# Kernel tuning notes

Hardware: AMD Instinct MI355X
Metric: run time of the kernel (lower is better)

## Reference

```python
import math
import jax, jax.numpy as jnp
import numpy as np

EPS = 1e-5
NUM_HEADS = 8

def gelu(x):
    return jax.nn.gelu(x, approximate=False)  # keras 'gelu' is exact

def layernorm(x, g, b):
    m = jnp.mean(x, axis=-1, keepdims=True)
    v = jnp.var(x, axis=-1, keepdims=True)
    return (x - m) * jax.lax.rsqrt(v + EPS) * g + b

def setup_inputs() -> dict:
    key = jax.random.key(0)
    ks = jax.random.split(key, 12)
    B, S, N, D = 2, 1, 2048, 256
    E = 256  # dim_emb == dim_out
    s_in = 1.0 / np.sqrt(D).astype(np.float32)
    s_e = 1.0 / np.sqrt(E).astype(np.float32)
    s_h = 1.0 / np.sqrt(4 * E).astype(np.float32)
    return {
        "X": jax.random.normal(ks[0], (B, S, N, D), jnp.float32),
        "Wq": jax.random.normal(ks[1], (D, E), jnp.float32) * s_in,
        "Wk": jax.random.normal(ks[2], (D, E), jnp.float32) * s_in,
        "Wv": jax.random.normal(ks[3], (D, E), jnp.float32) * s_in,
        "Wm": jax.random.normal(ks[4], (E, E), jnp.float32) * s_e,
        "bm": jnp.zeros((E,), jnp.float32),
        "W1": jax.random.normal(ks[5], (E, 4 * E), jnp.float32) * s_e,
        "bf1": jnp.zeros((4 * E,), jnp.float32),
        "W2": jax.random.normal(ks[6], (4 * E, E), jnp.float32) * s_h,
        "bf2": jnp.zeros((E,), jnp.float32),
        "ln0_g": jnp.ones((D,), jnp.float32),
        "ln0_b": jnp.zeros((D,), jnp.float32),
        "ln1_g": jnp.ones((E,), jnp.float32),
        "ln1_b": jnp.zeros((E,), jnp.float32),
    }

def reference(X, Wq, Wk, Wv, Wm, bm, W1, bf1, W2, bf2, ln0_g, ln0_b, ln1_g, ln1_b):
    B, S, N, D = X.shape  # S == 1 (set-transformer singleton axis)
    E = Wq.shape[1]
    H = NUM_HEADS
    dh = E // H
    dim_KV = D  # softmax scale uses dim_KV, not head dim (faithful to source)

    # pre-layer-norm applies only to the Q branch; K/V use raw X
    Xn = layernorm(X, ln0_g, ln0_b)
    Q = Xn @ Wq                      # (B,1,N,E)
    K = X @ Wk
    V = X @ Wv
    X_res = Q                        # fc_res is None -> residual is Q

    def to_heads(T):                 # (B,1,N,E) -> (B,H,N,dh), split along last dim
        return T[:, 0].reshape(B, N, H, dh).transpose(0, 2, 1, 3)

    q, k, v = to_heads(Q), to_heads(K), to_heads(V)
    A = jnp.einsum('bhnd,bhmd->bhnm', q, k) * (1.0 / math.sqrt(dim_KV))  # (B,H,N,N)
    P = jax.nn.softmax(A, axis=-1)
    mh = jnp.einsum('bhnm,bhmd->bhnd', P, v)            # (B,H,N,dh)
    mh = mh.transpose(0, 2, 1, 3).reshape(B, 1, N, E)   # concat heads on last dim

    Hm = gelu(mh @ Wm + bm)          # fc_mix_heads has gelu activation
    H_after_res = Hm + X_res
    H_rff = layernorm(H_after_res, ln1_g, ln1_b)

    # rff: Dense(4E, gelu) then an extra explicit gelu, then Dense(E, gelu)
    h1 = gelu(gelu(H_rff @ W1 + bf1))
    h2 = gelu(h1 @ W2 + bf2)
    return H_after_res + h2
```

## Files before the change

### kernel.cpp

```cpp
#include <hip/hip_runtime.h>
#include <math.h>

#define NTOK 2048
#define EDIM 256
#define ROWS 4096
#define SLOT (ROWS * EDIM)

typedef __attribute__((ext_vector_type(8))) short bf16x8;
typedef __attribute__((ext_vector_type(4))) short bf16x4_t;
typedef __attribute__((ext_vector_type(4))) unsigned short u16x4;
typedef __attribute__((ext_vector_type(4))) float f32x4;
typedef __attribute__((ext_vector_type(4))) unsigned u32x4;
typedef __attribute__((ext_vector_type(2))) unsigned u32x2;

__device__ __forceinline__ float gelu_f(float x) {
    return 0.5f * x * (1.0f + erff(x * 0.70710678118654752f));
}
__device__ __forceinline__ unsigned short f2bf(float x) {
    unsigned u = __builtin_bit_cast(unsigned, x);
    u += 0x7FFFu + ((u >> 16) & 1u);
    return (unsigned short)(u >> 16);
}
__device__ __forceinline__ float bf2f(unsigned short h) {
    unsigned u = ((unsigned)h) << 16;
    return __builtin_bit_cast(float, u);
}
__device__ __forceinline__ unsigned pack2(float lo, float hi) {
    unsigned r;
    asm("v_cvt_pk_bf16_f32 %0, %1, %2" : "=v"(r) : "v"(lo), "v"(hi));
    return r;
}

__global__ __launch_bounds__(256) void trans_w(const float* __restrict__ Wq, const float* __restrict__ Wk,
                                               const float* __restrict__ Wv, const float* __restrict__ Wm,
                                               const float* __restrict__ W1, const float* __restrict__ W2,
                                               unsigned short* WqT, unsigned short* WkvT,
                                               unsigned short* WmT, unsigned short* W1T,
                                               unsigned short* W2T) {
    __shared__ float Ls[64][65];
    const int bid = blockIdx.x;
    const float* src;
    unsigned short* dst;
    int K, N, t;
    if (bid < 16)       { src = Wq; dst = WqT;             K = 256;  N = 256;  t = bid; }
    else if (bid < 32)  { src = Wk; dst = WkvT;            K = 256;  N = 256;  t = bid - 16; }
    else if (bid < 48)  { src = Wv; dst = WkvT + 256*256;  K = 256;  N = 256;  t = bid - 32; }
    else if (bid < 64)  { src = Wm; dst = WmT;             K = 256;  N = 256;  t = bid - 48; }
    else if (bid < 128) { src = W1; dst = W1T;             K = 256;  N = 1024; t = bid - 64; }
    else                { src = W2; dst = W2T;             K = 1024; N = 256;  t = bid - 128; }
    const int tn = N >> 6;
    const int k0 = (t / tn) * 64, n0 = (t % tn) * 64;
    const int r = threadIdx.x >> 2, cq = threadIdx.x & 3;
#pragma unroll
    for (int u = 0; u < 4; ++u) {
        const float4 v = *(const float4*)&src[(size_t)(k0 + r) * N + n0 + cq * 16 + u * 4];
        Ls[r][cq * 16 + u * 4 + 0] = v.x;
        Ls[r][cq * 16 + u * 4 + 1] = v.y;
        Ls[r][cq * 16 + u * 4 + 2] = v.z;
        Ls[r][cq * 16 + u * 4 + 3] = v.w;
    }
    __syncthreads();
#pragma unroll
    for (int hh = 0; hh < 2; ++hh) {
        bf16x8 o;
#pragma unroll
        for (int j = 0; j < 8; ++j) o[j] = (short)f2bf(Ls[cq * 16 + hh * 8 + j][r]);
        *(bf16x8*)&dst[(size_t)(n0 + r) * K + k0 + cq * 16 + hh * 8] = o;
    }
}

template <bool RAW>
__global__ __launch_bounds__(256) void ln_bf16(const float* __restrict__ X, const float* __restrict__ g,
                                               const float* __restrict__ b, unsigned short* __restrict__ Y,
                                               unsigned short* __restrict__ Yraw) {
    const int wave = threadIdx.x >> 6, lane = threadIdx.x & 63;
    const int row = blockIdx.x * 4 + wave;
    const float4 v = *(const float4*)&X[(size_t)row * EDIM + lane * 4];
    float s = v.x + v.y + v.z + v.w;
    float s2 = v.x * v.x + v.y * v.y + v.z * v.z + v.w * v.w;
#pragma unroll
    for (int off = 1; off < 64; off <<= 1) {
        s += __shfl_xor(s, off);
        s2 += __shfl_xor(s2, off);
    }
    const float mean = s * (1.0f / 256.0f);
    const float var = s2 * (1.0f / 256.0f) - mean * mean;
    const float rstd = rsqrtf(var + 1e-5f);
    const float4 gg = *(const float4*)&g[lane * 4];
    const float4 bb = *(const float4*)&b[lane * 4];
    u16x4 o;
    o[0] = f2bf((v.x - mean) * rstd * gg.x + bb.x);
    o[1] = f2bf((v.y - mean) * rstd * gg.y + bb.y);
    o[2] = f2bf((v.z - mean) * rstd * gg.z + bb.z);
    o[3] = f2bf((v.w - mean) * rstd * gg.w + bb.w);
    *(u16x4*)&Y[(size_t)row * EDIM + lane * 4] = o;
    if (RAW) {
        u16x4 rw;
        rw[0] = f2bf(v.x); rw[1] = f2bf(v.y); rw[2] = f2bf(v.z); rw[3] = f2bf(v.w);
        *(u16x4*)&Yraw[(size_t)row * EDIM + lane * 4] = rw;
    }
}

template <int EPI, int BN>
__global__ __launch_bounds__(256) void gemm_bf16(const unsigned short* __restrict__ A,
                                                 const unsigned short* __restrict__ Bt,
                                                 const float* __restrict__ bias,
                                                 const float* __restrict__ res,
                                                 float* __restrict__ outF,
                                                 unsigned short* __restrict__ outB,
                                                 int M, int N, int K) {
    constexpr int NI = BN / 32;
    __shared__ unsigned short As[32][72];
    __shared__ unsigned short Bs[BN][72];
    const int tid = threadIdx.x;
    const int lane = tid & 63, wid = tid >> 6;
    const int c = lane & 15, g = lane >> 4;
    const int wm = wid & 1, wn = wid >> 1;
    const int row0 = blockIdx.y * 32, col0 = blockIdx.x * BN;
    const int sarow = tid >> 3, saq = tid & 7;
    f32x4 acc[NI] = {};
    for (int k0 = 0; k0 < K; k0 += 64) {
        __syncthreads();
        {
            const bf16x8 a0 = *(const bf16x8*)&A[(size_t)(row0 + sarow) * K + k0 + saq * 8];
            *(bf16x8*)&As[sarow][saq * 8] = a0;
            if (BN == 64) {
                const int sbrow = tid >> 2, sbq = tid & 3;
                const bf16x8* gb = (const bf16x8*)&Bt[(size_t)(col0 + sbrow) * K + k0 + sbq * 16];
                const bf16x8 b0 = gb[0], b1 = gb[1];
                *(bf16x8*)&Bs[sbrow][sbq * 16] = b0;
                *(bf16x8*)&Bs[sbrow][sbq * 16 + 8] = b1;
            } else {
                const bf16x8 b0 = *(const bf16x8*)&Bt[(size_t)(col0 + sarow) * K + k0 + saq * 8];
                *(bf16x8*)&Bs[sarow][saq * 8] = b0;
            }
        }
        __syncthreads();
#pragma unroll
        for (int ks = 0; ks < 2; ++ks) {
            const bf16x8 af = *(const bf16x8*)&As[wm * 16 + c][ks * 32 + 8 * g];
#pragma unroll
            for (int ni = 0; ni < NI; ++ni) {
                const bf16x8 bv = *(const bf16x8*)&Bs[(wn * NI + ni) * 16 + c][ks * 32 + 8 * g];
                acc[ni] = __builtin_amdgcn_mfma_f32_16x16x32_bf16(af, bv, acc[ni], 0, 0, 0);
            }
        }
    }
#pragma unroll
    for (int ni = 0; ni < NI; ++ni) {
        const int colx = col0 + (wn * NI + ni) * 16 + c;
        const float bi = (EPI != 0) ? bias[colx] : 0.0f;
#pragma unroll
        for (int r = 0; r < 4; ++r) {
            const int rowx = row0 + wm * 16 + 4 * g + r;
            const size_t idx = (size_t)rowx * N + colx;
            float v = acc[ni][r];
            if (EPI == 1) v = res[idx] + gelu_f(v + bi);
            else if (EPI == 2) v = gelu_f(gelu_f(v + bi));
            if (outF) outF[idx] = v;
            if (outB) outB[idx] = f2bf(v);
        }
    }
}

__global__ __launch_bounds__(256) void attn_mfma(const unsigned short* __restrict__ Qb,
                                                 const unsigned short* __restrict__ KVb,
                                                 unsigned short* __restrict__ Opart,
                                                 float* __restrict__ ML) {
    __shared__ char smem[18944];
    unsigned short (*Ks)[64][40] = (unsigned short (*)[64][40])smem;
    unsigned short (*Vt)[32][68] = (unsigned short (*)[32][68])(smem + 10240);
    float (*Otf)[16][36]         = (float (*)[16][36])smem;
    const int tid = threadIdx.x, lane = tid & 63, wid = tid >> 6;
    const int c = lane & 15, g = lane >> 4;
    const int bid = blockIdx.x;
    const int qt = bid & 31, h = (bid >> 5) & 7, b = (bid >> 8) & 1, s = bid >> 9;
    const int qrow = b * NTOK + qt * 64 + wid * 16;
    const int skey = tid >> 2, skq = tid & 3;
    const int vkp = tid & 31, vdq = tid >> 5;
    const int vk = (2 * vkp) & 31;
    const int vcol = ((2 * vkp) >> 5) * 32 + ((vk & 15) >> 2) * 8 + (vk >> 4) * 4 + (vk & 3);
    const size_t kvbase = (size_t)b * NTOK * 512 + h * 32;
    const int key0 = s * 512;

    bf16x8 qf;
    {
        const bf16x8 qraw = *(const bf16x8*)&Qb[(size_t)(qrow + c) * EDIM + h * 32 + 8 * g];
#pragma unroll
        for (int j = 0; j < 8; ++j)
            qf[j] = (short)f2bf(bf2f((unsigned short)qraw[j]) * 0.09016844f);
    }
    const f32x4 zero4 = {0.0f, 0.0f, 0.0f, 0.0f};
    f32x4 accO[2] = {zero4, zero4};
    float lsum = 0.0f;

    {
        const int c0 = key0;
        const bf16x8 kr = *(const bf16x8*)&KVb[kvbase + (size_t)(c0 + skey) * 512 + skq * 8];
        const u16x4 v0 = *(const u16x4*)&KVb[kvbase + (size_t)(c0 + 2 * vkp) * 512 + 256 + vdq * 4];
        const u16x4 v1 = *(const u16x4*)&KVb[kvbase + (size_t)(c0 + 2 * vkp + 1) * 512 + 256 + vdq * 4];
        *(bf16x8*)&Ks[0][skey][skq * 8] = kr;
#pragma unroll
        for (int i = 0; i < 4; ++i)
            *(unsigned*)&Vt[0][vdq * 4 + i][vcol] = ((unsigned)v1[i] << 16) | (unsigned)v0[i];
    }
    __syncthreads();

    for (int t = 0; t < 8; ++t) {
        const int cur = t & 1;
        bf16x8 kr2;
        u32x4 vr2;
        if (t < 7) {
            const int c0 = key0 + (t + 1) * 64;
            kr2 = *(const bf16x8*)&KVb[kvbase + (size_t)(c0 + skey) * 512 + skq * 8];
            const u16x4 v0 = *(const u16x4*)&KVb[kvbase + (size_t)(c0 + 2 * vkp) * 512 + 256 + vdq * 4];
            const u16x4 v1 = *(const u16x4*)&KVb[kvbase + (size_t)(c0 + 2 * vkp + 1) * 512 + 256 + vdq * 4];
#pragma unroll
            for (int i = 0; i < 4; ++i) vr2[i] = ((unsigned)v1[i] << 16) | (unsigned)v0[i];
        }

        f32x4 st[4];
        __builtin_amdgcn_s_setprio(1);
#pragma unroll
        for (int t4 = 0; t4 < 4; ++t4) {
            const bf16x8 kf = *(const bf16x8*)&Ks[cur][t4 * 16 + c][8 * g];
            st[t4] = __builtin_amdgcn_mfma_f32_16x16x32_bf16(kf, qf, zero4, 0, 0, 0);
        }
        __builtin_amdgcn_s_setprio(0);
#pragma unroll
        for (int t4 = 0; t4 < 4; ++t4)
#pragma unroll
            for (int r = 0; r < 4; ++r) {
                const float e = exp2f(st[t4][r]);
                st[t4][r] = e;
                lsum += e;
            }

        unsigned pk[8];
#pragma unroll
        for (int t4 = 0; t4 < 4; ++t4)
#pragma unroll
            for (int b2 = 0; b2 < 2; ++b2)
                pk[2 * t4 + b2] = pack2(st[t4][2 * b2], st[t4][2 * b2 + 1]);

        __builtin_amdgcn_s_setprio(1);
#pragma unroll
        for (int kc = 0; kc < 2; ++kc) {
            const u32x4 bw = {pk[4 * kc], pk[4 * kc + 1], pk[4 * kc + 2], pk[4 * kc + 3]};
            const bf16x8 bpv = __builtin_bit_cast(bf16x8, bw);
#pragma unroll
            for (int dt = 0; dt < 2; ++dt) {
                const bf16x4_t vlo = *(const bf16x4_t*)&Vt[cur][c + 16 * dt][8 * g + 32 * kc];
                const bf16x4_t vhi = *(const bf16x4_t*)&Vt[cur][c + 16 * dt][8 * g + 32 * kc + 4];
                const u32x2 L = __builtin_bit_cast(u32x2, vlo);
                const u32x2 H2 = __builtin_bit_cast(u32x2, vhi);
                const u32x4 q4 = {L[0], L[1], H2[0], H2[1]};
                const bf16x8 vf = __builtin_bit_cast(bf16x8, q4);
                accO[dt] = __builtin_amdgcn_mfma_f32_16x16x32_bf16(vf, bpv, accO[dt], 0, 0, 0);
            }
        }
        __builtin_amdgcn_s_setprio(0);

        if (t < 7) {
            *(bf16x8*)&Ks[cur ^ 1][skey][skq * 8] = kr2;
#pragma unroll
            for (int i = 0; i < 4; ++i)
                *(unsigned*)&Vt[cur ^ 1][vdq * 4 + i][vcol] = vr2[i];
            __syncthreads();
        }
    }

    lsum += __shfl_xor(lsum, 16);
    lsum += __shfl_xor(lsum, 32);
    __syncthreads();
    const float inv = 1.0f / lsum;
#pragma unroll
    for (int dt = 0; dt < 2; ++dt)
#pragma unroll
        for (int r = 0; r < 4; ++r)
            Otf[wid][c][dt * 16 + 4 * g + r] = accO[dt][r] * inv;
    if (g == 0) {
        ML[((size_t)s * 4096 + qrow + c) * 8 + h] = lsum;
    }
    const int oq = lane >> 2, odq = lane & 3;
    const float* srcp = &Otf[wid][oq][odq * 8];
    u32x4 packed;
    packed[0] = pack2(srcp[0], srcp[1]);
    packed[1] = pack2(srcp[2], srcp[3]);
    packed[2] = pack2(srcp[4], srcp[5]);
    packed[3] = pack2(srcp[6], srcp[7]);
    *(u32x4*)&Opart[(size_t)s * SLOT + (size_t)(qrow + oq) * EDIM + h * 32 + odq * 8] = packed;
}

__global__ __launch_bounds__(256) void attn_combine(const unsigned short* __restrict__ Opart,
                                                    const float* __restrict__ ML,
                                                    unsigned short* __restrict__ mhb) {
    const int flat4 = blockIdx.x * 256 + threadIdx.x;
    const int row = flat4 >> 6;
    const int col = (flat4 & 63) * 4;
    const int h = col >> 5;
    float lw[4];
    float lt = 0.0f;
#pragma unroll
    for (int s = 0; s < 4; ++s) {
        lw[s] = ML[((size_t)s * 4096 + row) * 8 + h];
        lt += lw[s];
    }
    const float inv = 1.0f / lt;
    float a[4] = {0.0f, 0.0f, 0.0f, 0.0f};
#pragma unroll
    for (int s = 0; s < 4; ++s) {
        const u16x4 p = *(const u16x4*)&Opart[(size_t)s * SLOT + (size_t)row * EDIM + col];
#pragma unroll
        for (int j = 0; j < 4; ++j) a[j] += lw[s] * bf2f((unsigned short)p[j]);
    }
    u16x4 r;
#pragma unroll
    for (int j = 0; j < 4; ++j) r[j] = f2bf(a[j] * inv);
    *(u16x4*)&mhb[(size_t)row * EDIM + col] = r;
}

extern "C" void kernel_launch(void* const* d_in, const int* in_sizes, int n_in,
                              void* d_out, int out_size, void* d_ws, size_t ws_size,
                              hipStream_t stream) {
    const float* X    = (const float*)d_in[0];
    const float* Wq   = (const float*)d_in[1];
    const float* Wk   = (const float*)d_in[2];
    const float* Wv   = (const float*)d_in[3];
    const float* Wm   = (const float*)d_in[4];
    const float* bm   = (const float*)d_in[5];
    const float* W1   = (const float*)d_in[6];
    const float* bf1  = (const float*)d_in[7];
    const float* W2   = (const float*)d_in[8];
    const float* bf2  = (const float*)d_in[9];
    const float* ln0g = (const float*)d_in[10];
    const float* ln0b = (const float*)d_in[11];
    const float* ln1g = (const float*)d_in[12];
    const float* ln1b = (const float*)d_in[13];
    float* out = (float*)d_out;
    char* w = (char*)d_ws;

    unsigned short* WqT  = (unsigned short*)(w + 0);
    unsigned short* WkvT = (unsigned short*)(w + 131072);
    unsigned short* WmT  = (unsigned short*)(w + 393216);
    unsigned short* W1T  = (unsigned short*)(w + 524288);
    unsigned short* W2T  = (unsigned short*)(w + 1048576);
    unsigned short* Xb   = (unsigned short*)(w + 1572864);
    float*          ML   = (float*)(w + 1572864);
    unsigned short* Xnb  = (unsigned short*)(w + 3670016);
    unsigned short* Qb   = (unsigned short*)(w + 5767168);
    float*          Qf   = (float*)(w + 7864320);
    unsigned short* KVb  = (unsigned short*)(w + 12058624);
    unsigned short* mhb  = (unsigned short*)(w + 16252928);
    float*          Hres = (float*)(w + 18350080);
    unsigned short* Hrff = (unsigned short*)(w + 22544384);
    unsigned short* h1b  = (unsigned short*)(w + 24641536);
    unsigned short* Opart= (unsigned short*)(w + 24641536);

    trans_w<<<192, 256, 0, stream>>>(Wq, Wk, Wv, Wm, W1, W2, WqT, WkvT, WmT, W1T, W2T);
    ln_bf16<true><<<ROWS / 4, 256, 0, stream>>>(X, ln0g, ln0b, Xnb, Xb);
    gemm_bf16<0, 32><<<dim3(8, 128), 256, 0, stream>>>(Xnb, WqT, nullptr, nullptr, Qf, Qb, ROWS, 256, 256);
    gemm_bf16<0, 64><<<dim3(8, 128), 256, 0, stream>>>(Xb, WkvT, nullptr, nullptr, nullptr, KVb, ROWS, 512, 256);
    attn_mfma<<<2048, 256, 0, stream>>>(Qb, KVb, Opart, ML);
    attn_combine<<<1024, 256, 0, stream>>>(Opart, ML, mhb);
    gemm_bf16<1, 32><<<dim3(8, 128), 256, 0, stream>>>(mhb, WmT, bm, Qf, Hres, nullptr, ROWS, 256, 256);
    ln_bf16<false><<<ROWS / 4, 256, 0, stream>>>(Hres, ln1g, ln1b, Hrff, nullptr);
    gemm_bf16<2, 64><<<dim3(16, 128), 256, 0, stream>>>(Hrff, W1T, bf1, nullptr, nullptr, h1b, ROWS, 1024, 256);
    gemm_bf16<1, 32><<<dim3(8, 128), 256, 0, stream>>>(h1b, W2T, bf2, Hres, out, nullptr, ROWS, 256, 1024);
}
```

Before: 92.03 us.

## Merge weight prep with LN0, fuse QKV GEMMs, register-prefetch GEMM tiles

Combines the weight transpose/convert kernel and the first layernorm into one launch. It also merges the Q and KV projection GEMMs into a single launch with a grid split by blockIdx.y. The shared GEMM body now prefetches the next K-tile into registers while computing the current one, and moves one barrier to the end of the loop. The aim is fewer kernel launches and less exposed global-load latency, at the cost of extra register pressure and a larger static LDS footprint for the Q blocks.

Measured after the change: 86.89 us. 1.06x faster.

```diff
diff --git a/kernel.cpp b/kernel.cpp
--- a/kernel.cpp
+++ b/kernel.cpp
@@ -31,41 +31,72 @@
     return r;
 }
 
-__global__ __launch_bounds__(256) void trans_w(const float* __restrict__ Wq, const float* __restrict__ Wk,
-                                               const float* __restrict__ Wv, const float* __restrict__ Wm,
-                                               const float* __restrict__ W1, const float* __restrict__ W2,
-                                               unsigned short* WqT, unsigned short* WkvT,
-                                               unsigned short* WmT, unsigned short* W1T,
-                                               unsigned short* W2T) {
+__global__ __launch_bounds__(256) void prep(const float* __restrict__ Wq, const float* __restrict__ Wk,
+                                            const float* __restrict__ Wv, const float* __restrict__ Wm,
+                                            const float* __restrict__ W1, const float* __restrict__ W2,
+                                            const float* __restrict__ X, const float* __restrict__ ln0g,
+                                            const float* __restrict__ ln0b,
+                                            unsigned short* WqT, unsigned short* WkvT,
+                                            unsigned short* WmT, unsigned short* W1T,
+                                            unsigned short* W2T,
+                                            unsigned short* __restrict__ Xnb,
+                                            unsigned short* __restrict__ Xb) {
     __shared__ float Ls[64][65];
     const int bid = blockIdx.x;
-    const float* src;
-    unsigned short* dst;
-    int K, N, t;
-    if (bid < 16)       { src = Wq; dst = WqT;             K = 256;  N = 256;  t = bid; }
-    else if (bid < 32)  { src = Wk; dst = WkvT;            K = 256;  N = 256;  t = bid - 16; }
-    else if (bid < 48)  { src = Wv; dst = WkvT + 256*256;  K = 256;  N = 256;  t = bid - 32; }
-    else if (bid < 64)  { src = Wm; dst = WmT;             K = 256;  N = 256;  t = bid - 48; }
-    else if (bid < 128) { src = W1; dst = W1T;             K = 256;  N = 1024; t = bid - 64; }
-    else                { src = W2; dst = W2T;             K = 1024; N = 256;  t = bid - 128; }
-    const int tn = N >> 6;
-    const int k0 = (t / tn) * 64, n0 = (t % tn) * 64;
-    const int r = threadIdx.x >> 2, cq = threadIdx.x & 3;
-#pragma unroll
-    for (int u = 0; u < 4; ++u) {
-        const float4 v = *(const float4*)&src[(size_t)(k0 + r) * N + n0 + cq * 16 + u * 4];
-        Ls[r][cq * 16 + u * 4 + 0] = v.x;
-        Ls[r][cq * 16 + u * 4 + 1] = v.y;
-        Ls[r][cq * 16 + u * 4 + 2] = v.z;
-        Ls[r][cq * 16 + u * 4 + 3] = v.w;
-    }
-    __syncthreads();
-#pragma unroll
-    for (int hh = 0; hh < 2; ++hh) {
-        bf16x8 o;
-#pragma unroll
-        for (int j = 0; j < 8; ++j) o[j] = (short)f2bf(Ls[cq * 16 + hh * 8 + j][r]);
-        *(bf16x8*)&dst[(size_t)(n0 + r) * K + k0 + cq * 16 + hh * 8] = o;
+    if (bid < 192) {
+        const float* src;
+        unsigned short* dst;
+        int K, N, t;
+        if (bid < 16)       { src = Wq; dst = WqT;             K = 256;  N = 256;  t = bid; }
+        else if (bid < 32)  { src = Wk; dst = WkvT;            K = 256;  N = 256;  t = bid - 16; }
+        else if (bid < 48)  { src = Wv; dst = WkvT + 256*256;  K = 256;  N = 256;  t = bid - 32; }
+        else if (bid < 64)  { src = Wm; dst = WmT;             K = 256;  N = 256;  t = bid - 48; }
+        else if (bid < 128) { src = W1; dst = W1T;             K = 256;  N = 1024; t = bid - 64; }
+        else                { src = W2; dst = W2T;             K = 1024; N = 256;  t = bid - 128; }
+        const int tn = N >> 6;
+        const int k0 = (t / tn) * 64, n0 = (t % tn) * 64;
+        const int r = threadIdx.x >> 2, cq = threadIdx.x & 3;
+#pragma unroll
+        for (int u = 0; u < 4; ++u) {
+            const float4 v = *(const float4*)&src[(size_t)(k0 + r) * N + n0 + cq * 16 + u * 4];
+            Ls[r][cq * 16 + u * 4 + 0] = v.x;
+            Ls[r][cq * 16 + u * 4 + 1] = v.y;
+            Ls[r][cq * 16 + u * 4 + 2] = v.z;
+            Ls[r][cq * 16 + u * 4 + 3] = v.w;
+        }
+        __syncthreads();
+#pragma unroll
+        for (int hh = 0; hh < 2; ++hh) {
+            bf16x8 o;
+#pragma unroll
+            for (int j = 0; j < 8; ++j) o[j] = (short)f2bf(Ls[cq * 16 + hh * 8 + j][r]);
+            *(bf16x8*)&dst[(size_t)(n0 + r) * K + k0 + cq * 16 + hh * 8] = o;
+        }
+    } else {
+        const int wave = threadIdx.x >> 6, lane = threadIdx.x & 63;
+        const int row = (bid - 192) * 4 + wave;
+        const float4 v = *(const float4*)&X[(size_t)row * EDIM + lane * 4];
+        float s = v.x + v.y + v.z + v.w;
+        float s2 = v.x * v.x + v.y * v.y + v.z * v.z + v.w * v.w;
+#pragma unroll
+        for (int off = 1; off < 64; off <<= 1) {
+            s += __shfl_xor(s, off);
+            s2 += __shfl_xor(s2, off);
+        }
+        const float mean = s * (1.0f / 256.0f);
+        const float var = s2 * (1.0f / 256.0f) - mean * mean;
+        const float rstd = rsqrtf(var + 1e-5f);
+        const float4 gg = *(const float4*)&ln0g[lane * 4];
+        const float4 bb = *(const float4*)&ln0b[lane * 4];
+        u16x4 o;
+        o[0] = f2bf((v.x - mean) * rstd * gg.x + bb.x);
+        o[1] = f2bf((v.y - mean) * rstd * gg.y + bb.y);
+        o[2] = f2bf((v.z - mean) * rstd * gg.z + bb.z);
+        o[3] = f2bf((v.w - mean) * rstd * gg.w + bb.w);
+        *(u16x4*)&Xnb[(size_t)row * EDIM + lane * 4] = o;
+        u16x4 rw;
+        rw[0] = f2bf(v.x); rw[1] = f2bf(v.y); rw[2] = f2bf(v.z); rw[3] = f2bf(v.w);
+        *(u16x4*)&Xb[(size_t)row * EDIM + lane * 4] = rw;
     }
 }
 
@@ -102,40 +133,51 @@
 }
 
 template <int EPI, int BN>
-__global__ __launch_bounds__(256) void gemm_bf16(const unsigned short* __restrict__ A,
-                                                 const unsigned short* __restrict__ Bt,
-                                                 const float* __restrict__ bias,
-                                                 const float* __restrict__ res,
-                                                 float* __restrict__ outF,
-                                                 unsigned short* __restrict__ outB,
-                                                 int M, int N, int K) {
+__device__ __forceinline__ void gemm_body(const unsigned short* __restrict__ A,
+                                          const unsigned short* __restrict__ Bt,
+                                          const float* __restrict__ bias,
+                                          const float* __restrict__ res,
+                                          float* __restrict__ outF,
+                                          unsigned short* __restrict__ outB,
+                                          int N, int K, int bx, int by,
+                                          unsigned short (*As)[72], unsigned short (*Bs)[72]) {
     constexpr int NI = BN / 32;
-    __shared__ unsigned short As[32][72];
-    __shared__ unsigned short Bs[BN][72];
     const int tid = threadIdx.x;
     const int lane = tid & 63, wid = tid >> 6;
     const int c = lane & 15, g = lane >> 4;
     const int wm = wid & 1, wn = wid >> 1;
-    const int row0 = blockIdx.y * 32, col0 = blockIdx.x * BN;
+    const int row0 = by * 32, col0 = bx * BN;
     const int sarow = tid >> 3, saq = tid & 7;
+    const int sbrow = tid >> 2, sbq = tid & 3;
     f32x4 acc[NI] = {};
+    bf16x8 a_r = *(const bf16x8*)&A[(size_t)(row0 + sarow) * K + saq * 8];
+    bf16x8 b_r0, b_r1;
+    if (BN == 64) {
+        const bf16x8* gb = (const bf16x8*)&Bt[(size_t)(col0 + sbrow) * K + sbq * 16];
+        b_r0 = gb[0];
+        b_r1 = gb[1];
+    } else {
+        b_r0 = *(const bf16x8*)&Bt[(size_t)(col0 + sarow) * K + saq * 8];
+    }
     for (int k0 = 0; k0 < K; k0 += 64) {
+        *(bf16x8*)&As[sarow][saq * 8] = a_r;
+        if (BN == 64) {
+            *(bf16x8*)&Bs[sbrow][sbq * 16] = b_r0;
+            *(bf16x8*)&Bs[sbrow][sbq * 16 + 8] = b_r1;
+        } else {
+            *(bf16x8*)&Bs[sarow][saq * 8] = b_r0;
+        }
         __syncthreads();
-        {
-            const bf16x8 a0 = *(const bf16x8*)&A[(size_t)(row0 + sarow) * K + k0 + saq * 8];
-            *(bf16x8*)&As[sarow][saq * 8] = a0;
+        if (k0 + 64 < K) {
+            a_r = *(const bf16x8*)&A[(size_t)(row0 + sarow) * K + k0 + 64 + saq * 8];
             if (BN == 64) {
-                const int sbrow = tid >> 2, sbq = tid & 3;
-                const bf16x8* gb = (const bf16x8*)&Bt[(size_t)(col0 + sbrow) * K + k0 + sbq * 16];
-                const bf16x8 b0 = gb[0], b1 = gb[1];
-                *(bf16x8*)&Bs[sbrow][sbq * 16] = b0;
-                *(bf16x8*)&Bs[sbrow][sbq * 16 + 8] = b1;
+                const bf16x8* gb = (const bf16x8*)&Bt[(size_t)(col0 + sbrow) * K + k0 + 64 + sbq * 16];
+                b_r0 = gb[0];
+                b_r1 = gb[1];
             } else {
-                const bf16x8 b0 = *(const bf16x8*)&Bt[(size_t)(col0 + sarow) * K + k0 + saq * 8];
-                *(bf16x8*)&Bs[sarow][saq * 8] = b0;
+                b_r0 = *(const bf16x8*)&Bt[(size_t)(col0 + sarow) * K + k0 + 64 + saq * 8];
             }
         }
-        __syncthreads();
 #pragma unroll
         for (int ks = 0; ks < 2; ++ks) {
             const bf16x8 af = *(const bf16x8*)&As[wm * 16 + c][ks * 32 + 8 * g];
@@ -145,6 +187,7 @@
                 acc[ni] = __builtin_amdgcn_mfma_f32_16x16x32_bf16(af, bv, acc[ni], 0, 0, 0);
             }
         }
+        __syncthreads();
     }
 #pragma unroll
     for (int ni = 0; ni < NI; ++ni) {
@@ -161,6 +204,34 @@
             if (outB) outB[idx] = f2bf(v);
         }
     }
+}
+
+template <int EPI, int BN>
+__global__ __launch_bounds__(256) void gemm_bf16(const unsigned short* __restrict__ A,
+                                                 const unsigned short* __restrict__ Bt,
+                                                 const float* __restrict__ bias,
+                                                 const float* __restrict__ res,
+                                                 float* __restrict__ outF,
+                                                 unsigned short* __restrict__ outB,
+                                                 int M, int N, int K) {
+    __shared__ unsigned short As[32][72];
+    __shared__ unsigned short Bs[BN][72];
+    gemm_body<EPI, BN>(A, Bt, bias, res, outF, outB, N, K, blockIdx.x, blockIdx.y, As, Bs);
+}
+
+__global__ __launch_bounds__(256) void qkv_gemm(const unsigned short* __restrict__ Xnb,
+                                                const unsigned short* __restrict__ Xb,
+                                                const unsigned short* __restrict__ WqT,
+                                                const unsigned short* __restrict__ WkvT,
+                                                float* __restrict__ Qf,
+                                                unsigned short* __restrict__ Qb,
+                                                unsigned short* __restrict__ KVb) {
+    __shared__ unsigned short As[32][72];
+    __shared__ unsigned short Bs[64][72];
+    if (blockIdx.y < 128)
+        gemm_body<0, 32>(Xnb, WqT, nullptr, nullptr, Qf, Qb, 256, 256, blockIdx.x, blockIdx.y, As, Bs);
+    else
+        gemm_body<0, 64>(Xb, WkvT, nullptr, nullptr, nullptr, KVb, 512, 256, blockIdx.x, blockIdx.y - 128, As, Bs);
 }
 
 __global__ __launch_bounds__(256) void attn_mfma(const unsigned short* __restrict__ Qb,
@@ -357,10 +428,9 @@
     unsigned short* h1b  = (unsigned short*)(w + 24641536);
     unsigned short* Opart= (unsigned short*)(w + 24641536);
 
-    trans_w<<<192, 256, 0, stream>>>(Wq, Wk, Wv, Wm, W1, W2, WqT, WkvT, WmT, W1T, W2T);
-    ln_bf16<true><<<ROWS / 4, 256, 0, stream>>>(X, ln0g, ln0b, Xnb, Xb);
-    gemm_bf16<0, 32><<<dim3(8, 128), 256, 0, stream>>>(Xnb, WqT, nullptr, nullptr, Qf, Qb, ROWS, 256, 256);
-    gemm_bf16<0, 64><<<dim3(8, 128), 256, 0, stream>>>(Xb, WkvT, nullptr, nullptr, nullptr, KVb, ROWS, 512, 256);
+    prep<<<1216, 256, 0, stream>>>(Wq, Wk, Wv, Wm, W1, W2, X, ln0g, ln0b,
+                                   WqT, WkvT, WmT, W1T, W2T, Xnb, Xb);
+    qkv_gemm<<<dim3(8, 256), 256, 0, stream>>>(Xnb, Xb, WqT, WkvT, Qf, Qb, KVb);
     attn_mfma<<<2048, 256, 0, stream>>>(Qb, KVb, Opart, ML);
     attn_combine<<<1024, 256, 0, stream>>>(Opart, ML, mhb);
     gemm_bf16<1, 32><<<dim3(8, 128), 256, 0, stream>>>(mhb, WmT, bm, Qf, Hres, nullptr, ROWS, 256, 256);
```
